# Kernel optimization log

Hardware: AMD Instinct MI355X
Metric: run time of the kernel (lower is better)

## Reference

```python
import jax, jax.numpy as jnp
import numpy as np

B, N, C = 2, 2048, 768
H = 12
D = C // H
SCALE = D ** -0.5
EPS = 1e-5
HID = 4 * C


def layer_norm(x, g, b):
    mu = jnp.mean(x, axis=-1, keepdims=True)
    var = jnp.var(x, axis=-1, keepdims=True)
    return (x - mu) * jax.lax.rsqrt(var + EPS) * g + b


def setup_inputs():
    key = jax.random.key(0)
    ks = jax.random.split(key, 12)
    s = C ** -0.5
    x = jax.random.normal(ks[0], (B, N, C), dtype=jnp.float32)
    mask = (jax.random.uniform(ks[1], (B, N, N)) < 0.1).astype(jnp.float32)
    return {
        "x": x,
        "mask": mask,
        "g1": jnp.ones((C,), jnp.float32),
        "b1": jnp.zeros((C,), jnp.float32),
        "Wq": jax.random.normal(ks[2], (C, C), jnp.float32) * s,
        "Wkv": jax.random.normal(ks[3], (2 * C, C), jnp.float32) * s,
        "Wp": jax.random.normal(ks[4], (C, C), jnp.float32) * s,
        "bp": jnp.zeros((C,), jnp.float32),
        "g2": jnp.ones((C,), jnp.float32),
        "b2": jnp.zeros((C,), jnp.float32),
        "W1": jax.random.normal(ks[5], (HID, C), jnp.float32) * s,
        "bf1": jnp.zeros((HID,), jnp.float32),
        "W2": jax.random.normal(ks[6], (C, HID), jnp.float32) * (HID ** -0.5),
        "bf2": jnpmp if False else jnp.zeros((C,), jnp.float32),
    }


def block_fwd(x, mask, g1, b1, Wq, Wkv, Wp, bp, g2, b2, W1, bf1, W2, bf2):
    # --- attention branch (pre-norm) ---
    xn = layer_norm(x, g1, b1)
    q = (xn @ Wq.T).reshape(B, N, H, D).transpose(0, 2, 1, 3)      # bhnd
    kv = (xn @ Wkv.T).reshape(B, N, 2, H, D).transpose(2, 0, 3, 1, 4)
    k, v = kv[0], kv[1]                                             # bhnd
    attn = jnp.einsum('bhnd,bhmd->bhnm', q, k) * SCALE
    attn = attn + (mask * -100000.0)[:, None]                       # additive mask
    attn = jax.nn.softmax(attn, axis=-1)
    o = jnp.einsum('bhnm,bhmd->bhnd', attn, v)
    o = o.transpose(0, 2, 1, 3).reshape(B, N, C)
    o = o @ Wp.T + bp
    x = x + o
    # --- MLP branch (pre-norm) ---
    xn2 = layer_norm(x, g2, b2)
    h = jax.nn.gelu(xn2 @ W1.T + bf1, approximate=False)
    x = x + (h @ W2.T + bf2)
    return x


def reference(x, mask, g1, b1, Wq, Wkv, Wp, bp, g2, b2, W1, bf1, W2, bf2):
    return block_fwd(x, mask, g1, b1, Wq, Wkv, Wp, bp, g2, b2, W1, bf1, W2, bf2)
```

## Files before the change

kernel.cpp:

```cpp
#include <hip/hip_runtime.h>
#include <hip/hip_bf16.h>
#include <cstdint>
#include <cstddef>

#define BB 2
#define NN 2048
#define CC 768
#define HH 12
#define DD 64
#define HID 3072
#define TT (BB*NN)

typedef __attribute__((ext_vector_type(8))) short bf16x8;
typedef __attribute__((ext_vector_type(4))) short bf16x4;
typedef __attribute__((ext_vector_type(4))) float f32x4;

__device__ __forceinline__ unsigned short f2bf(float f) {
    unsigned int u = __float_as_uint(f);
    u += 0x7fffu + ((u >> 16) & 1u);
    return (unsigned short)(u >> 16);
}
__device__ __forceinline__ float bf2f(unsigned short u) {
    return __uint_as_float(((unsigned int)u) << 16);
}
#if __has_builtin(__builtin_amdgcn_exp2f)
#define EXP2F(x) __builtin_amdgcn_exp2f(x)
#else
#define EXP2F(x) exp2f(x)
#endif

__device__ __forceinline__ void gload16(const void* g, void* l) {
    __builtin_amdgcn_global_load_lds((__attribute__((address_space(1))) unsigned int*)g,
                                     (__attribute__((address_space(3))) unsigned int*)l,
                                     16, 0, 0);
}

#define WAITV(N) asm volatile("s_waitcnt vmcnt(" #N ")" ::: "memory")
#define WAITLGKM asm volatile("s_waitcnt lgkmcnt(0)" ::: "memory")

struct CvtArgs {
    const float* in[5];
    unsigned short* out[5];
    int n4[5];
};
typedef __attribute__((ext_vector_type(4))) float float4v;
typedef __attribute__((ext_vector_type(4))) unsigned short ushort4v;
__global__ __launch_bounds__(256) void cvt5_kernel(CvtArgs a) {
    int base = blockIdx.x * 256 + threadIdx.x;
    int stride = gridDim.x * 256;
#pragma unroll
    for (int s = 0; s < 5; ++s) {
        const float4v* ip = (const float4v*)a.in[s];
        ushort4v* op = (ushort4v*)a.out[s];
        for (int i = base; i < a.n4[s]; i += stride) {
            float4v v = ip[i];
            ushort4v o;
            o[0] = f2bf(v[0]); o[1] = f2bf(v[1]); o[2] = f2bf(v[2]); o[3] = f2bf(v[3]);
            op[i] = o;
        }
    }
}

__global__ __launch_bounds__(256) void maskbits_kernel(const float* __restrict__ mask,
                                                       unsigned short* __restrict__ mb, int n) {
    int i = blockIdx.x * 256 + threadIdx.x;
    if (i >= n) return;
    const float4v* mp = (const float4v*)(mask + (size_t)i * 16);
    unsigned int bits = 0;
#pragma unroll
    for (int q = 0; q < 4; ++q) {
        float4v v = mp[q];
#pragma unroll
        for (int j = 0; j < 4; ++j) bits |= (v[j] > 0.5f) ? (1u << (q * 4 + j)) : 0u;
    }
    mb[i] = (unsigned short)bits;
}

__global__ __launch_bounds__(256) void ln_kernel(const float* __restrict__ x,
                                                 const float* __restrict__ g,
                                                 const float* __restrict__ b,
                                                 unsigned short* __restrict__ out) {
    int t = blockIdx.x;
    int tid = threadIdx.x;
    const float* xr = x + (size_t)t * CC;
    float v0 = xr[tid], v1 = xr[tid + 256], v2 = xr[tid + 512];
    float s = v0 + v1 + v2;
    float s2 = v0 * v0 + v1 * v1 + v2 * v2;
#pragma unroll
    for (int off = 1; off < 64; off <<= 1) {
        s  += __shfl_xor(s, off);
        s2 += __shfl_xor(s2, off);
    }
    __shared__ float red[8];
    int wv = tid >> 6, lane = tid & 63;
    if (lane == 0) { red[wv] = s; red[wv + 4] = s2; }
    __syncthreads();
    s  = red[0] + red[1] + red[2] + red[3];
    s2 = red[4] + red[5] + red[6] + red[7];
    float mu   = s * (1.0f / CC);
    float var  = s2 * (1.0f / CC) - mu * mu;
    float rstd = rsqrtf(var + 1e-5f);
    unsigned short* orow = out + (size_t)t * CC;
    orow[tid]       = f2bf((v0 - mu) * rstd * g[tid]       + b[tid]);
    orow[tid + 256] = f2bf((v1 - mu) * rstd * g[tid + 256] + b[tid + 256]);
    orow[tid + 512] = f2bf((v2 - mu) * rstd * g[tid + 512] + b[tid + 512]);
}

template <int EPI, int BM>
__global__ __launch_bounds__(256) void gemm_bt(const unsigned short* __restrict__ A,
                                               const unsigned short* __restrict__ Bw,
                                               const float* __restrict__ bias,
                                               const float* __restrict__ res,
                                               void* __restrict__ out,
                                               int M, int N, int K) {
    constexpr int MI  = BM / 32;
    constexpr int NCA = BM / 64;
    constexpr int NCB = 2;
    __shared__ alignas(16) unsigned short As[3][BM * 32];
    __shared__ alignas(16) unsigned short Bs[3][128 * 32];
    int tid = threadIdx.x;
    int lane = tid & 63, wv = tid >> 6;
    int l16 = lane & 15, lg = lane >> 4;

    int BMT = M / BM, chunk = BMT >> 3;
    int id = blockIdx.x;
    int xcd = id & 7, r = id >> 3;
    int bm = xcd * chunk + (r % chunk);
    int bn = r / chunk;

    int wm = (wv & 1) * (BM / 2), wn = (wv >> 1) * 64;

    const unsigned short* Ab = A + (size_t)bm * BM * K;
    const unsigned short* Bb = Bw + (size_t)bn * 128 * K;

    const unsigned short* aSrc[NCA]; int aDst[NCA];
#pragma unroll
    for (int i = 0; i < NCA; ++i) {
        int c = tid + i * 256;
        int row = c >> 2, p = c & 3;
        int lc = p ^ ((row >> 1) & 3);
        aSrc[i] = Ab + (size_t)row * K + lc * 8;
        aDst[i] = c * 8;
    }
    const unsigned short* bSrc[NCB]; int bDst[NCB];
#pragma unroll
    for (int i = 0; i < NCB; ++i) {
        int c = tid + i * 256;
        int row = c >> 2, p = c & 3;
        int lc = p ^ ((row >> 1) & 3);
        bSrc[i] = Bb + (size_t)row * K + lc * 8;
        bDst[i] = c * 8;
    }
    int aoff = (wm + l16) * 32 + ((lg ^ (((wm + l16) >> 1) & 3)) * 8);
    int boff = (wn + l16) * 32 + ((lg ^ (((wn + l16) >> 1) & 3)) * 8);

    f32x4 acc[MI][4];
#pragma unroll
    for (int i = 0; i < MI; ++i)
#pragma unroll
        for (int j = 0; j < 4; ++j) acc[i][j] = f32x4{0.f, 0.f, 0.f, 0.f};

    auto STAGE = [&](int s, int k0) {
#pragma unroll
        for (int i = 0; i < NCA; ++i) gload16(aSrc[i] + k0, &As[s][aDst[i]]);
#pragma unroll
        for (int i = 0; i < NCB; ++i) gload16(bSrc[i] + k0, &Bs[s][bDst[i]]);
    };

    STAGE(0, 0);
    STAGE(1, 32);
    int nt = K / 32;
    for (int t = 0; t < nt; ++t) {
        int cur = t % 3;
        if (t + 1 < nt) {
            if constexpr (BM == 128) { WAITV(4); } else { WAITV(3); }
        } else {
            WAITV(0);
        }
        WAITLGKM;
        __builtin_amdgcn_s_barrier();
        if (t + 2 < nt) STAGE((t + 2) % 3, (t + 2) * 32);
        bf16x8 af[MI], bfr[4];
#pragma unroll
        for (int mi = 0; mi < MI; ++mi) af[mi]  = *(const bf16x8*)&As[cur][aoff + mi * 512];
#pragma unroll
        for (int ni = 0; ni < 4; ++ni)  bfr[ni] = *(const bf16x8*)&Bs[cur][boff + ni * 512];
#pragma unroll
        for (int mi = 0; mi < MI; ++mi)
#pragma unroll
            for (int ni = 0; ni < 4; ++ni)
                acc[mi][ni] = __builtin_amdgcn_mfma_f32_16x16x32_bf16(bfr[ni], af[mi], acc[mi][ni], 0, 0, 0);
    }

#pragma unroll
    for (int mi = 0; mi < MI; ++mi) {
        int row = bm * BM + wm + mi * 16 + l16;
#pragma unroll
        for (int ni = 0; ni < 4; ++ni) {
            int col = bn * 128 + wn + ni * 16 + lg * 4;
            size_t idx = (size_t)row * N + col;
            f32x4 v = acc[mi][ni];
            if (EPI == 0) {
                bf16x4 ov;
#pragma unroll
                for (int r2 = 0; r2 < 4; ++r2) ov[r2] = (short)f2bf(v[r2]);
                *(bf16x4*)((unsigned short*)out + idx) = ov;
            } else if (EPI == 1 || EPI == 3) {
                f32x4 bv = *(const f32x4*)&bias[col];
                f32x4 rv = *(const f32x4*)&res[idx];
                f32x4 ov;
#pragma unroll
                for (int r2 = 0; r2 < 4; ++r2) ov[r2] = v[r2] + bv[r2] + rv[r2];
                *(f32x4*)((float*)out + idx) = ov;
            } else {
                f32x4 bv = *(const f32x4*)&bias[col];
                bf16x4 ov;
#pragma unroll
                for (int r2 = 0; r2 < 4; ++r2) {
                    float t2 = v[r2] + bv[r2];
                    t2 = 0.5f * t2 * (1.0f + erff(t2 * 0.70710678118f));
                    ov[r2] = (short)f2bf(t2);
                }
                *(bf16x4*)((unsigned short*)out + idx) = ov;
            }
        }
    }
}

#define KVB 64
#define ANT (NN/KVB)
#define VP 68
__global__ __launch_bounds__(256, 4) void attn_kernel(const unsigned short* __restrict__ qkv,
                                                      const unsigned short* __restrict__ maskb,
                                                      unsigned short* __restrict__ o) {
    __shared__ alignas(16) unsigned short Ks[2][64 * 64];
    __shared__ alignas(16) unsigned short Vt[2][64 * VP];
    int tid = threadIdx.x;
    int lane = tid & 63, wv = tid >> 6;
    int l16 = lane & 15, lg = lane >> 4;
    int id = blockIdx.x;
    int xcd = id & 7, r = id >> 3;
    int bh = xcd * 3 + (r % 3);
    int qb = r / 3;
    int b = bh / HH, h = bh % HH;
    int qrow = qb * 64 + wv * 16 + l16;

    const unsigned short* qp = qkv + ((size_t)(b * NN + qrow)) * 2304 + h * DD;
    bf16x8 q0r = *(const bf16x8*)(qp + 8 * lg);
    bf16x8 q1r = *(const bf16x8*)(qp + 32 + 8 * lg);
    const float QSC = 0.125f * 1.4426950408889634f;
    bf16x8 q0, q1;
#pragma unroll
    for (int j = 0; j < 8; ++j) {
        q0[j] = (short)f2bf(bf2f((unsigned short)q0r[j]) * QSC);
        q1[j] = (short)f2bf(bf2f((unsigned short)q1r[j]) * QSC);
    }

    const unsigned short* mrow  = maskb + ((size_t)(b * NN + qrow)) * 128;
    const unsigned short* kbase = qkv + (size_t)b * NN * 2304 + 768 + h * DD;
    const unsigned short* vbase = qkv + (size_t)b * NN * 2304 + 1536 + h * DD;

    const unsigned short* kSrc[2]; int kDst[2];
#pragma unroll
    for (int i = 0; i < 2; ++i) {
        int c = tid + i * 256;
        int row = c >> 3, p = c & 7;
        int lc = p ^ (row & 7);
        kSrc[i] = kbase + (size_t)row * 2304 + lc * 8;
        kDst[i] = c * 8;
    }
    int kp = tid & 31, dg = tid >> 5;
    const unsigned short* vSrc = vbase + (size_t)(2 * kp) * 2304 + dg * 8;

    int sw = l16 & 7;
    int kb0 = l16 * 64 + ((lg ^ sw) * 8);
    int kb1 = l16 * 64 + (((lg + 4) ^ sw) * 8);
    int vbo = l16 * VP + lg * 4;

    bf16x8 va, vb;
    unsigned long long mb_cur, mb_nxt;

    f32x4 oa[4];
#pragma unroll
    for (int i = 0; i < 4; ++i) oa[i] = f32x4{0.f, 0.f, 0.f, 0.f};
    float mrun = -INFINITY, lrun = 0.f;

    auto LOAD = [&](int t, int s) {
#pragma unroll
        for (int i = 0; i < 2; ++i) gload16(kSrc[i] + (size_t)t * KVB * 2304, &Ks[s][kDst[i]]);
        const unsigned short* vp = vSrc + (size_t)t * KVB * 2304;
        va = *(const bf16x8*)(vp);
        vb = *(const bf16x8*)(vp + 2304);
        mb_nxt = *(const unsigned long long*)(mrow + t * 4);
    };
    auto WRITEV = [&](int s) {
        unsigned int* VtU = (unsigned int*)Vt[s];
#pragma unroll
        for (int j = 0; j < 8; ++j)
            VtU[(dg * 8 + j) * (VP / 2) + kp] =
                (unsigned int)(unsigned short)va[j] | ((unsigned int)(unsigned short)vb[j] << 16);
    };

    LOAD(0, 0);
    WRITEV(0);
    mb_cur = mb_nxt;
    __syncthreads();
    int cur = 0;

    for (int kt = 0; kt < ANT; ++kt) {
        bool pre = (kt + 1 < ANT);
        if (pre) LOAD(kt + 1, cur ^ 1);
        const unsigned short* Ksc = Ks[cur];
        const unsigned short* Vtc = Vt[cur];

        float sv[16];
#pragma unroll
        for (int ks = 0; ks < 4; ++ks) {
            bf16x8 k0 = *(const bf16x8*)&Ksc[kb0 + ks * 1024];
            bf16x8 k1 = *(const bf16x8*)&Ksc[kb1 + ks * 1024];
            f32x4 sa = f32x4{0.f, 0.f, 0.f, 0.f};
            sa = __builtin_amdgcn_mfma_f32_16x16x32_bf16(k0, q0, sa, 0, 0, 0);
            sa = __builtin_amdgcn_mfma_f32_16x16x32_bf16(k1, q1, sa, 0, 0, 0);
            unsigned int m16 = (unsigned int)(mb_cur >> (ks * 16 + lg * 4));
#pragma unroll
            for (int r2 = 0; r2 < 4; ++r2) {
                float mbit = (float)((m16 >> r2) & 1u);
                sv[ks * 4 + r2] = fmaf(mbit, -144269.5f, sa[r2]);
            }
        }
        float tmax = sv[0];
#pragma unroll
        for (int i = 1; i < 16; ++i) tmax = fmaxf(tmax, sv[i]);
        tmax = fmaxf(tmax, __shfl_xor(tmax, 16));
        tmax = fmaxf(tmax, __shfl_xor(tmax, 32));

        if (__any(tmax > mrun + 11.5f)) {
            float mnew = fmaxf(mrun, tmax);
            float sc = EXP2F(mrun - mnew);
            lrun *= sc;
#pragma unroll
            for (int db = 0; db < 4; ++db) {
                oa[db][0] *= sc; oa[db][1] *= sc; oa[db][2] *= sc; oa[db][3] *= sc;
            }
            mrun = mnew;
        }

        float ps = 0.f;
        bf16x4 pf[4];
#pragma unroll
        for (int ks = 0; ks < 4; ++ks)
#pragma unroll
            for (int r2 = 0; r2 < 4; ++r2) {
                float p = EXP2F(sv[ks * 4 + r2] - mrun);
                ps += p;
                pf[ks][r2] = (short)f2bf(p);
            }
        lrun += ps;

#pragma unroll
        for (int ks = 0; ks < 4; ++ks)
#pragma unroll
            for (int db = 0; db < 4; ++db) {
                bf16x4 vf = *(const bf16x4*)&Vtc[vbo + db * 16 * VP + ks * 16];
                oa[db] = __builtin_amdgcn_mfma_f32_16x16x16bf16_1k(vf, pf[ks], oa[db], 0, 0, 0);
            }

        if (pre) WRITEV(cur ^ 1);
        __syncthreads();
        if (pre) { cur ^= 1; mb_cur = mb_nxt; }
    }

    float lt = lrun;
    lt += __shfl_xor(lt, 16);
    lt += __shfl_xor(lt, 32);
    float inv = 1.0f / lt;
    unsigned short* op = o + ((size_t)(b * NN + qrow)) * CC + h * DD;
#pragma unroll
    for (int db = 0; db < 4; ++db) {
        bf16x4 ov;
#pragma unroll
        for (int r2 = 0; r2 < 4; ++r2) ov[r2] = (short)f2bf(oa[db][r2] * inv);
        *(bf16x4*)&op[db * 16 + lg * 4] = ov;
    }
}

extern "C" void kernel_launch(void* const* d_in, const int* in_sizes, int n_in,
                              void* d_out, int out_size, void* d_ws, size_t ws_size,
                              hipStream_t stream) {
    const float* x    = (const float*)d_in[0];
    const float* mask = (const float*)d_in[1];
    const float* g1   = (const float*)d_in[2];
    const float* b1   = (const float*)d_in[3];
    const float* Wq   = (const float*)d_in[4];
    const float* Wkv  = (const float*)d_in[5];
    const float* Wp   = (const float*)d_in[6];
    const float* bp   = (const float*)d_in[7];
    const float* g2   = (const float*)d_in[8];
    const float* b2   = (const float*)d_in[9];
    const float* W1   = (const float*)d_in[10];
    const float* bf1  = (const float*)d_in[11];
    const float* W2   = (const float*)d_in[12];
    const float* bf2  = (const float*)d_in[13];
    float* out = (float*)d_out;

    char* w = (char*)d_ws;
    unsigned short* wqkv = (unsigned short*)w;      w += (size_t)2304 * 768 * 2;
    unsigned short* wp   = (unsigned short*)w;      w += (size_t)768 * 768 * 2;
    unsigned short* w1   = (unsigned short*)w;      w += (size_t)3072 * 768 * 2;
    unsigned short* w2   = (unsigned short*)w;      w += (size_t)768 * 3072 * 2;
    unsigned short* xn   = (unsigned short*)w;      w += (size_t)TT * CC * 2;
    unsigned short* qkv  = (unsigned short*)w;      w += (size_t)TT * 2304 * 2;
    unsigned short* mb   = (unsigned short*)w;      w += (size_t)BB * NN * 128 * 2;
    unsigned short* obuf = (unsigned short*)w;      w += (size_t)TT * CC * 2;
    float*          x1   = (float*)w;               w += (size_t)TT * CC * 4;
    unsigned short* xn2  = (unsigned short*)w;      w += (size_t)TT * CC * 2;
    unsigned short* hbuf = (unsigned short*)w;      w += (size_t)TT * HID * 2;

    CvtArgs ca;
    ca.in[0] = Wq;  ca.out[0] = wqkv;             ca.n4[0] = 768 * 768 / 4;
    ca.in[1] = Wkv; ca.out[1] = wqkv + 768 * 768; ca.n4[1] = 1536 * 768 / 4;
    ca.in[2] = Wp;  ca.out[2] = wp;               ca.n4[2] = 768 * 768 / 4;
    ca.in[3] = W1;  ca.out[3] = w1;               ca.n4[3] = 3072 * 768 / 4;
    ca.in[4] = W2;  ca.out[4] = w2;               ca.n4[4] = 768 * 3072 / 4;
    cvt5_kernel<<<1024, 256, 0, stream>>>(ca);

    {
        int n = BB * NN * (NN / 16);
        maskbits_kernel<<<(n + 255) / 256, 256, 0, stream>>>(mask, mb, n);
    }

    ln_kernel<<<TT, 256, 0, stream>>>(x, g1, b1, xn);

    gemm_bt<0, 128><<<32 * 18, 256, 0, stream>>>(xn, wqkv, nullptr, nullptr, qkv, TT, 2304, 768);

    attn_kernel<<<32 * 24, 256, 0, stream>>>(qkv, mb, obuf);

    gemm_bt<1, 64><<<64 * 6, 256, 0, stream>>>(obuf, wp, bp, x, x1, TT, 768, 768);

    ln_kernel<<<TT, 256, 0, stream>>>(x1, g2, b2, xn2);

    gemm_bt<2, 128><<<32 * 24, 256, 0, stream>>>(xn2, w1, bf1, nullptr, hbuf, TT, HID, 768);

    gemm_bt<3, 64><<<64 * 6, 256, 0, stream>>>(hbuf, w2, bf2, x1, out, TT, 768, HID);
}
```

Baseline: 222.9 us.

## Retile GEMMs to 128x64 double-buffered tiles and split-K the MLP down-projection

```diff
diff --git a/kernel.cpp b/kernel.cpp
--- a/kernel.cpp
+++ b/kernel.cpp
@@ -80,7 +80,7 @@
                                                  const float* __restrict__ g,
                                                  const float* __restrict__ b,
                                                  unsigned short* __restrict__ out) {
-    int t = blockIdx.x;
+    int t = ((blockIdx.x & 7) << 9) | (blockIdx.x >> 3);
     int tid = threadIdx.x;
     const float* xr = x + (size_t)t * CC;
     float v0 = xr[tid], v1 = xr[tid + 256], v2 = xr[tid + 512];
@@ -106,98 +106,94 @@
     orow[tid + 512] = f2bf((v2 - mu) * rstd * g[tid + 512] + b[tid + 512]);
 }
 
-template <int EPI, int BM>
-__global__ __launch_bounds__(256) void gemm_bt(const unsigned short* __restrict__ A,
-                                               const unsigned short* __restrict__ Bw,
-                                               const float* __restrict__ bias,
-                                               const float* __restrict__ res,
-                                               void* __restrict__ out,
-                                               int M, int N, int K) {
-    constexpr int MI  = BM / 32;
-    constexpr int NCA = BM / 64;
-    constexpr int NCB = 2;
-    __shared__ alignas(16) unsigned short As[3][BM * 32];
-    __shared__ alignas(16) unsigned short Bs[3][128 * 32];
+template <int EPI>
+__global__ __launch_bounds__(256, 6) void gemm_bt(const unsigned short* __restrict__ A,
+                                                  const unsigned short* __restrict__ Bw,
+                                                  const float* __restrict__ bias,
+                                                  const float* __restrict__ res,
+                                                  void* __restrict__ out,
+                                                  int M, int N, int lda, int ldb, int K) {
+    __shared__ alignas(16) unsigned short As[2][128 * 32];
+    __shared__ alignas(16) unsigned short Bs[2][64 * 32];
     int tid = threadIdx.x;
     int lane = tid & 63, wv = tid >> 6;
     int l16 = lane & 15, lg = lane >> 4;
 
-    int BMT = M / BM, chunk = BMT >> 3;
+    int BMT = M >> 7, chunk = BMT >> 3;
     int id = blockIdx.x;
     int xcd = id & 7, r = id >> 3;
     int bm = xcd * chunk + (r % chunk);
     int bn = r / chunk;
 
-    int wm = (wv & 1) * (BM / 2), wn = (wv >> 1) * 64;
-
-    const unsigned short* Ab = A + (size_t)bm * BM * K;
-    const unsigned short* Bb = Bw + (size_t)bn * 128 * K;
-
-    const unsigned short* aSrc[NCA]; int aDst[NCA];
-#pragma unroll
-    for (int i = 0; i < NCA; ++i) {
+    int wm = wv * 32;
+
+    const unsigned short* Ab = A + (size_t)bm * 128 * lda;
+    const unsigned short* Bb = Bw + (size_t)bn * 64 * ldb;
+
+    const unsigned short* aSrc[2]; int aDst[2];
+#pragma unroll
+    for (int i = 0; i < 2; ++i) {
         int c = tid + i * 256;
         int row = c >> 2, p = c & 3;
         int lc = p ^ ((row >> 1) & 3);
-        aSrc[i] = Ab + (size_t)row * K + lc * 8;
+        aSrc[i] = Ab + (size_t)row * lda + lc * 8;
         aDst[i] = c * 8;
     }
-    const unsigned short* bSrc[NCB]; int bDst[NCB];
-#pragma unroll
-    for (int i = 0; i < NCB; ++i) {
-        int c = tid + i * 256;
+    const unsigned short* bSrc; int bDst;
+    {
+        int c = tid;
         int row = c >> 2, p = c & 3;
         int lc = p ^ ((row >> 1) & 3);
-        bSrc[i] = Bb + (size_t)row * K + lc * 8;
-        bDst[i] = c * 8;
-    }
-    int aoff = (wm + l16) * 32 + ((lg ^ (((wm + l16) >> 1) & 3)) * 8);
-    int boff = (wn + l16) * 32 + ((lg ^ (((wn + l16) >> 1) & 3)) * 8);
-
-    f32x4 acc[MI][4];
-#pragma unroll
-    for (int i = 0; i < MI; ++i)
+        bSrc = Bb + (size_t)row * ldb + lc * 8;
+        bDst = c * 8;
+    }
+    int arow = wm + l16;
+    int aoff = arow * 32 + ((lg ^ ((arow >> 1) & 3)) * 8);
+    int boff = l16 * 32 + ((lg ^ ((l16 >> 1) & 3)) * 8);
+
+    f32x4 acc[2][4];
+#pragma unroll
+    for (int i = 0; i < 2; ++i)
 #pragma unroll
         for (int j = 0; j < 4; ++j) acc[i][j] = f32x4{0.f, 0.f, 0.f, 0.f};
 
     auto STAGE = [&](int s, int k0) {
 #pragma unroll
-        for (int i = 0; i < NCA; ++i) gload16(aSrc[i] + k0, &As[s][aDst[i]]);
-#pragma unroll
-        for (int i = 0; i < NCB; ++i) gload16(bSrc[i] + k0, &Bs[s][bDst[i]]);
+        for (int i = 0; i < 2; ++i) gload16(aSrc[i] + k0, &As[s][aDst[i]]);
+        gload16(bSrc + k0, &Bs[s][bDst]);
     };
 
     STAGE(0, 0);
-    STAGE(1, 32);
     int nt = K / 32;
     for (int t = 0; t < nt; ++t) {
-        int cur = t % 3;
+        int cur = t & 1;
         if (t + 1 < nt) {
-            if constexpr (BM == 128) { WAITV(4); } else { WAITV(3); }
+            STAGE(cur ^ 1, (t + 1) * 32);
+            WAITV(3);
         } else {
             WAITV(0);
         }
+        __builtin_amdgcn_s_barrier();
+        bf16x8 af[2], bfr[4];
+#pragma unroll
+        for (int mi = 0; mi < 2; ++mi) af[mi]  = *(const bf16x8*)&As[cur][aoff + mi * 512];
+#pragma unroll
+        for (int ni = 0; ni < 4; ++ni)  bfr[ni] = *(const bf16x8*)&Bs[cur][boff + ni * 512];
+#pragma unroll
+        for (int mi = 0; mi < 2; ++mi)
+#pragma unroll
+            for (int ni = 0; ni < 4; ++ni)
+                acc[mi][ni] = __builtin_amdgcn_mfma_f32_16x16x32_bf16(bfr[ni], af[mi], acc[mi][ni], 0, 0, 0);
         WAITLGKM;
         __builtin_amdgcn_s_barrier();
-        if (t + 2 < nt) STAGE((t + 2) % 3, (t + 2) * 32);
-        bf16x8 af[MI], bfr[4];
-#pragma unroll
-        for (int mi = 0; mi < MI; ++mi) af[mi]  = *(const bf16x8*)&As[cur][aoff + mi * 512];
-#pragma unroll
-        for (int ni = 0; ni < 4; ++ni)  bfr[ni] = *(const bf16x8*)&Bs[cur][boff + ni * 512];
-#pragma unroll
-        for (int mi = 0; mi < MI; ++mi)
-#pragma unroll
-            for (int ni = 0; ni < 4; ++ni)
-                acc[mi][ni] = __builtin_amdgcn_mfma_f32_16x16x32_bf16(bfr[ni], af[mi], acc[mi][ni], 0, 0, 0);
-    }
-
-#pragma unroll
-    for (int mi = 0; mi < MI; ++mi) {
-        int row = bm * BM + wm + mi * 16 + l16;
+    }
+
+#pragma unroll
+    for (int mi = 0; mi < 2; ++mi) {
+        int row = bm * 128 + wm + mi * 16 + l16;
 #pragma unroll
         for (int ni = 0; ni < 4; ++ni) {
-            int col = bn * 128 + wn + ni * 16 + lg * 4;
+            int col = bn * 64 + ni * 16 + lg * 4;
             size_t idx = (size_t)row * N + col;
             f32x4 v = acc[mi][ni];
             if (EPI == 0) {
@@ -205,14 +201,14 @@
 #pragma unroll
                 for (int r2 = 0; r2 < 4; ++r2) ov[r2] = (short)f2bf(v[r2]);
                 *(bf16x4*)((unsigned short*)out + idx) = ov;
-            } else if (EPI == 1 || EPI == 3) {
+            } else if (EPI == 1) {
                 f32x4 bv = *(const f32x4*)&bias[col];
                 f32x4 rv = *(const f32x4*)&res[idx];
                 f32x4 ov;
 #pragma unroll
                 for (int r2 = 0; r2 < 4; ++r2) ov[r2] = v[r2] + bv[r2] + rv[r2];
                 *(f32x4*)((float*)out + idx) = ov;
-            } else {
+            } else if (EPI == 2) {
                 f32x4 bv = *(const f32x4*)&bias[col];
                 bf16x4 ov;
 #pragma unroll
@@ -222,8 +218,27 @@
                     ov[r2] = (short)f2bf(t2);
                 }
                 *(bf16x4*)((unsigned short*)out + idx) = ov;
+            } else {
+                *(f32x4*)((float*)out + idx) = v;
             }
         }
+    }
+}
+
+__global__ __launch_bounds__(256) void addred_kernel(float* __restrict__ out,
+                                                     const float* __restrict__ p1,
+                                                     const float* __restrict__ p2, int n4) {
+    int i = blockIdx.x * 256 + threadIdx.x;
+    int s = gridDim.x * 256;
+    f32x4* o4 = (f32x4*)out;
+    const f32x4* a4 = (const f32x4*)p1;
+    const f32x4* b4 = (const f32x4*)p2;
+    for (; i < n4; i += s) {
+        f32x4 a = o4[i], b = a4[i], c = b4[i];
+        f32x4 ov;
+#pragma unroll
+        for (int j = 0; j < 4; ++j) ov[j] = a[j] + b[j] + c[j];
+        o4[i] = ov;
     }
 }
 
@@ -408,6 +423,7 @@
     unsigned short* wp   = (unsigned short*)w;      w += (size_t)768 * 768 * 2;
     unsigned short* w1   = (unsigned short*)w;      w += (size_t)3072 * 768 * 2;
     unsigned short* w2   = (unsigned short*)w;      w += (size_t)768 * 3072 * 2;
+    char* xn_region = w;
     unsigned short* xn   = (unsigned short*)w;      w += (size_t)TT * CC * 2;
     unsigned short* qkv  = (unsigned short*)w;      w += (size_t)TT * 2304 * 2;
     unsigned short* mb   = (unsigned short*)w;      w += (size_t)BB * NN * 128 * 2;
@@ -416,6 +432,9 @@
     unsigned short* xn2  = (unsigned short*)w;      w += (size_t)TT * CC * 2;
     unsigned short* hbuf = (unsigned short*)w;      w += (size_t)TT * HID * 2;
 
+    float* part1 = (float*)xn_region;
+    float* part2 = part1 + (size_t)TT * CC;
+
     CvtArgs ca;
     ca.in[0] = Wq;  ca.out[0] = wqkv;             ca.n4[0] = 768 * 768 / 4;
     ca.in[1] = Wkv; ca.out[1] = wqkv + 768 * 768; ca.n4[1] = 1536 * 768 / 4;
@@ -431,15 +450,24 @@
 
     ln_kernel<<<TT, 256, 0, stream>>>(x, g1, b1, xn);
 
-    gemm_bt<0, 128><<<32 * 18, 256, 0, stream>>>(xn, wqkv, nullptr, nullptr, qkv, TT, 2304, 768);
+    gemm_bt<0><<<32 * 36, 256, 0, stream>>>(xn, wqkv, nullptr, nullptr, qkv,
+                                            TT, 2304, 768, 768, 768);
 
     attn_kernel<<<32 * 24, 256, 0, stream>>>(qkv, mb, obuf);
 
-    gemm_bt<1, 64><<<64 * 6, 256, 0, stream>>>(obuf, wp, bp, x, x1, TT, 768, 768);
+    gemm_bt<1><<<32 * 12, 256, 0, stream>>>(obuf, wp, bp, x, x1,
+                                            TT, 768, 768, 768, 768);
 
     ln_kernel<<<TT, 256, 0, stream>>>(x1, g2, b2, xn2);
 
-    gemm_bt<2, 128><<<32 * 24, 256, 0, stream>>>(xn2, w1, bf1, nullptr, hbuf, TT, HID, 768);
-
-    gemm_bt<3, 64><<<64 * 6, 256, 0, stream>>>(hbuf, w2, bf2, x1, out, TT, 768, HID);
-}
+    gemm_bt<2><<<32 * 48, 256, 0, stream>>>(xn2, w1, bf1, nullptr, hbuf,
+                                            TT, HID, 768, 768, 768);
+
+    gemm_bt<1><<<32 * 12, 256, 0, stream>>>(hbuf,        w2,        bf2, x1, out,
+                                            TT, 768, 3072, 3072, 1024);
+    gemm_bt<4><<<32 * 12, 256, 0, stream>>>(hbuf + 1024, w2 + 1024, nullptr, nullptr, part1,
+                                            TT, 768, 3072, 3072, 1024);
+    gemm_bt<4><<<32 * 12, 256, 0, stream>>>(hbuf + 2048, w2 + 2048, nullptr, nullptr, part2,
+                                            TT, 768, 3072, 3072, 1024);
+    addred_kernel<<<1024, 256, 0, stream>>>(out, part1, part2, TT * CC / 4);
+}
```

New measurement: 243.3 us. 1.09x slower.
